# Optimization experiments

Hardware: AMD Instinct MI355X
Metric: run time of the kernel (lower is better)

Reference implementation:

```python
import jax, jax.numpy as jnp
import numpy as np
import math

N, C3, T = 32, 192, 2048  # C3 = 3 * head_dim

def setup_inputs() -> dict:
    key = jax.random.key(0)
    qkv = jax.random.normal(key, (N, C3, T), dtype=jnp.float32)
    return {"qkv": qkv}

def reference(qkv):
    ch = qkv.shape[1] // 3
    q, k, v = jnp.split(qkv, 3, axis=1)              # each [N, C, T]
    scale = 1.0 / math.sqrt(math.sqrt(ch))           # applied to both q and k
    # [N, T, T] attention scores
    weight = jnp.einsum('bct,bcs->bts', q * scale, k * scale)
    weight = jax.nn.softmax(weight.astype(jnp.float32), axis=-1).astype(qkv.dtype)
    # [N, C, T] output
    return jnp.einsum('bts,bcs->bct', weight, v)
```

## Files before the change

kernel.cpp:

```cpp
#include <hip/hip_runtime.h>

#define T_DIM 2048
#define NB 32

#define QT_OFF 0
#define KB_OFF 4194304
#define VB_OFF 8388608

typedef _Float16 half8 __attribute__((ext_vector_type(8)));
typedef _Float16 half4 __attribute__((ext_vector_type(4)));
typedef float f32x16 __attribute__((ext_vector_type(16)));
typedef float f32x4 __attribute__((ext_vector_type(4)));

#define ZERO16 (f32x16){0.f,0.f,0.f,0.f,0.f,0.f,0.f,0.f,0.f,0.f,0.f,0.f,0.f,0.f,0.f,0.f}

__global__ __launch_bounds__(256) void prepass(const float* __restrict__ qkv,
                                               _Float16* __restrict__ ws) {
  const int ttile = blockIdx.x;
  const int b = blockIdx.y;
  const int type = blockIdx.z;
  const int t0 = ttile * 64;
  __shared__ float Ls[64][65];

  const int tid = threadIdx.x;
  const int cc = tid >> 4;
  const int tt = (tid & 15) << 2;
  const float QS = 0.125f * 1.4426950408889634f;
  const float* src = qkv + ((size_t)b * 192 + type * 64) * T_DIM;
#pragma unroll
  for (int p = 0; p < 4; ++p) {
    const int c = p * 16 + cc;
    float4 v = *(const float4*)&src[(size_t)c * T_DIM + t0 + tt];
    if (type == 0) { v.x *= QS; v.y *= QS; v.z *= QS; v.w *= QS; }
    Ls[c][tt] = v.x; Ls[c][tt + 1] = v.y; Ls[c][tt + 2] = v.z; Ls[c][tt + 3] = v.w;
  }
  __syncthreads();

  if (type == 0) {
    const int t = tid >> 2, cg = (tid & 3) * 16;
    half8 h0, h1;
#pragma unroll
    for (int j = 0; j < 8; ++j) h0[j] = (_Float16)Ls[cg + j][t];
#pragma unroll
    for (int j = 0; j < 8; ++j) h1[j] = (_Float16)Ls[cg + 8 + j][t];
    _Float16* dst = ws + QT_OFF + ((size_t)b * T_DIM + t0 + t) * 64 + cg;
    *(half8*)dst = h0;
    *(half8*)(dst + 8) = h1;
  } else if (type == 1) {
    const int f = tid >> 6, h = (tid >> 5) & 1, s31 = tid & 31;
#pragma unroll
    for (int sbl = 0; sbl < 2; ++sbl) {
      const int sb = (t0 >> 5) + sbl;
      half8 hv;
#pragma unroll
      for (int j = 0; j < 8; ++j) hv[j] = (_Float16)Ls[f * 16 + h * 8 + j][sbl * 32 + s31];
      _Float16* dst = ws + KB_OFF + ((size_t)b * 64 + sb) * 2048 + f * 512 + h * 256 + s31 * 8;
      *(half8*)dst = hv;
    }
  } else {
#pragma unroll
    for (int p = 0; p < 2; ++p) {
      const int g = p * 256 + tid;
      const int sgl = g >> 6, c = g & 63;
      half8 hv;
#pragma unroll
      for (int j = 0; j < 8; ++j) hv[j] = (_Float16)Ls[c][sgl * 8 + j];
      _Float16* dst = ws + VB_OFF + (((size_t)b * 256 + (t0 >> 3) + sgl) * 64 + c) * 8;
      *(half8*)dst = hv;
    }
  }
}

__global__ __launch_bounds__(256, 4) void qkv_main(const _Float16* __restrict__ ws,
                                                   float* __restrict__ out) {
  const int tid = threadIdx.x;
  const int wave = tid >> 6, lane = tid & 63;
  const int l31 = lane & 31, h = lane >> 5;
  const int qh = wave & 1;
  const int kh = wave >> 1;
  const int b = blockIdx.x & 31;
  const int qg = blockIdx.x >> 5;
  const int t0 = qg * 64 + qh * 32;

  __shared__ float cl[2][64][36];

  const _Float16* kbase = ws + KB_OFF + (size_t)b * 131072 + (size_t)kh * 65536;
  const _Float16* vbase = ws + VB_OFF + (size_t)b * 131072 + (size_t)kh * 65536;

  const _Float16* qp = ws + QT_OFF + ((size_t)b * T_DIM + t0 + l31) * 64 + h * 8;
  half8 bq[4];
#pragma unroll
  for (int f = 0; f < 4; ++f) bq[f] = *(const half8*)(qp + f * 16);

  f32x16 o0 = ZERO16, o1 = ZERO16;
  float lp = 0.f;

  const _Float16* kp = kbase + h * 256 + l31 * 8;
  const _Float16* vp = vbase + l31 * 8 + h * 4;

  half8 ak0 = *(const half8*)(kp);
  half8 ak1 = *(const half8*)(kp + 512);
  half8 ak2 = *(const half8*)(kp + 1024);
  half8 ak3 = *(const half8*)(kp + 1536);

  for (int sb = 0; sb < 32; ++sb) {
    const size_t off = (size_t)(sb + 1 < 32 ? sb + 1 : sb) * 2048;
    half8 nk0 = *(const half8*)(kp + off);
    half8 nk1 = *(const half8*)(kp + off + 512);
    half8 nk2 = *(const half8*)(kp + off + 1024);
    half8 nk3 = *(const half8*)(kp + off + 1536);
    const _Float16* vpi = vp + (size_t)sb * 2048;
    half4 bv[8];
#pragma unroll
    for (int g = 0; g < 4; ++g) {
      bv[2 * g] = *(const half4*)(vpi + g * 512);
      bv[2 * g + 1] = *(const half4*)(vpi + g * 512 + 256);
    }

    f32x16 s = ZERO16;
    s = __builtin_amdgcn_mfma_f32_32x32x16_f16(ak0, bq[0], s, 0, 0, 0);
    s = __builtin_amdgcn_mfma_f32_32x32x16_f16(ak1, bq[1], s, 0, 0, 0);
    s = __builtin_amdgcn_mfma_f32_32x32x16_f16(ak2, bq[2], s, 0, 0, 0);
    s = __builtin_amdgcn_mfma_f32_32x32x16_f16(ak3, bq[3], s, 0, 0, 0);

    half4 ap[4];
    float lp0 = 0.f, lp1 = 0.f;
#pragma unroll
    for (int g = 0; g < 4; ++g) {
      const float e0 = __builtin_amdgcn_exp2f(s[4 * g + 0]);
      const float e1 = __builtin_amdgcn_exp2f(s[4 * g + 1]);
      const float e2 = __builtin_amdgcn_exp2f(s[4 * g + 2]);
      const float e3 = __builtin_amdgcn_exp2f(s[4 * g + 3]);
      lp0 += e0 + e1;
      lp1 += e2 + e3;
      ap[g] = (half4){(_Float16)e0, (_Float16)e1, (_Float16)e2, (_Float16)e3};
    }
    lp += lp0 + lp1;

#pragma unroll
    for (int g = 0; g < 4; ++g) {
      o0 = __builtin_amdgcn_mfma_f32_32x32x8f16(ap[g], bv[2 * g], o0, 0, 0, 0);
      o1 = __builtin_amdgcn_mfma_f32_32x32x8f16(ap[g], bv[2 * g + 1], o1, 0, 0, 0);
    }

    ak0 = nk0; ak1 = nk1; ak2 = nk2; ak3 = nk3;
  }

  if (kh == 1) {
#pragma unroll
    for (int g = 0; g < 4; ++g) {
      *(f32x4*)&cl[qh][lane][g * 4] =
          (f32x4){o0[4 * g], o0[4 * g + 1], o0[4 * g + 2], o0[4 * g + 3]};
      *(f32x4*)&cl[qh][lane][16 + g * 4] =
          (f32x4){o1[4 * g], o1[4 * g + 1], o1[4 * g + 2], o1[4 * g + 3]};
    }
    cl[qh][lane][32] = lp;
  }
  __syncthreads();
  if (kh == 0) {
#pragma unroll
    for (int g = 0; g < 4; ++g) {
      const f32x4 p0 = *(const f32x4*)&cl[qh][lane][g * 4];
      const f32x4 p1 = *(const f32x4*)&cl[qh][lane][16 + g * 4];
#pragma unroll
      for (int j = 0; j < 4; ++j) {
        o0[4 * g + j] += p0[j];
        o1[4 * g + j] += p1[j];
      }
    }
    lp += cl[qh][lane][32];
    const float lf = lp + __shfl_xor(lp, 32);
    const float linv = 1.0f / lf;
    float* ob = out + (size_t)b * 64 * T_DIM + t0;
#pragma unroll
    for (int g = 0; g < 4; ++g) {
      f32x4 r0, r1;
#pragma unroll
      for (int j = 0; j < 4; ++j) {
        const float il = __shfl(linv, g * 8 + h * 4 + j);
        r0[j] = o0[g * 4 + j] * il;
        r1[j] = o1[g * 4 + j] * il;
      }
      const int q = g * 8 + h * 4;
      *(f32x4*)&ob[(size_t)l31 * T_DIM + q] = r0;
      *(f32x4*)&ob[(size_t)(32 + l31) * T_DIM + q] = r1;
    }
  }
}

extern "C" void kernel_launch(void* const* d_in, const int* in_sizes, int n_in,
                              void* d_out, int out_size, void* d_ws, size_t ws_size,
                              hipStream_t stream) {
  const float* qkv = (const float*)d_in[0];
  float* out = (float*)d_out;
  _Float16* ws = (_Float16*)d_ws;
  hipLaunchKernelGGL(prepass, dim3(32, 32, 3), dim3(256), 0, stream, qkv, ws);
  hipLaunchKernelGGL(qkv_main, dim3(1024), dim3(256), 0, stream, ws, out);
}
```

Measured before the change: 141.5 us.

## Use K=16 MFMA for PV product with cross-half shuffles and prefetch V

Replaces the eight 32x32x8 f16 MFMAs in the P·V product with four 32x32x16 MFMAs per iteration. The probability fragments are regrouped across lane halves with xor-32 shuffles so they match the wider K layout, and V is read as half8 with a new offset pattern. V loads are also double-buffered alongside K one iteration ahead, and the loop is unrolled by two. This cuts MFMA issue count and overlaps V loads with compute, at the cost of extra shuffles and higher register pressure under the occupancy-4 launch bound.

```diff
diff --git a/kernel.cpp b/kernel.cpp
--- a/kernel.cpp
+++ b/kernel.cpp
@@ -11,8 +11,16 @@
 typedef _Float16 half4 __attribute__((ext_vector_type(4)));
 typedef float f32x16 __attribute__((ext_vector_type(16)));
 typedef float f32x4 __attribute__((ext_vector_type(4)));
+typedef int i32x2 __attribute__((ext_vector_type(2)));
 
 #define ZERO16 (f32x16){0.f,0.f,0.f,0.f,0.f,0.f,0.f,0.f,0.f,0.f,0.f,0.f,0.f,0.f,0.f,0.f}
+
+__device__ __forceinline__ half4 shflx32(half4 v) {
+  i32x2 i = __builtin_bit_cast(i32x2, v);
+  i.x = __shfl_xor(i.x, 32);
+  i.y = __shfl_xor(i.y, 32);
+  return __builtin_bit_cast(half4, i);
+}
 
 __global__ __launch_bounds__(256) void prepass(const float* __restrict__ qkv,
                                                _Float16* __restrict__ ws) {
@@ -96,32 +104,34 @@
   float lp = 0.f;
 
   const _Float16* kp = kbase + h * 256 + l31 * 8;
-  const _Float16* vp = vbase + l31 * 8 + h * 4;
-
-  half8 ak0 = *(const half8*)(kp);
-  half8 ak1 = *(const half8*)(kp + 512);
-  half8 ak2 = *(const half8*)(kp + 1024);
-  half8 ak3 = *(const half8*)(kp + 1536);
-
+  const _Float16* vp = vbase + h * 512 + l31 * 8;
+
+  half8 ak[2][4], av[2][4];
+#pragma unroll
+  for (int f = 0; f < 4; ++f) ak[0][f] = *(const half8*)(kp + f * 512);
+  av[0][0] = *(const half8*)(vp);
+  av[0][1] = *(const half8*)(vp + 256);
+  av[0][2] = *(const half8*)(vp + 1024);
+  av[0][3] = *(const half8*)(vp + 1280);
+
+#pragma unroll 2
   for (int sb = 0; sb < 32; ++sb) {
-    const size_t off = (size_t)(sb + 1 < 32 ? sb + 1 : sb) * 2048;
-    half8 nk0 = *(const half8*)(kp + off);
-    half8 nk1 = *(const half8*)(kp + off + 512);
-    half8 nk2 = *(const half8*)(kp + off + 1024);
-    half8 nk3 = *(const half8*)(kp + off + 1536);
-    const _Float16* vpi = vp + (size_t)sb * 2048;
-    half4 bv[8];
-#pragma unroll
-    for (int g = 0; g < 4; ++g) {
-      bv[2 * g] = *(const half4*)(vpi + g * 512);
-      bv[2 * g + 1] = *(const half4*)(vpi + g * 512 + 256);
-    }
+    const int cur = sb & 1, nxt = cur ^ 1;
+    const size_t noff = (size_t)(sb + 1 < 32 ? sb + 1 : sb) * 2048;
+    ak[nxt][0] = *(const half8*)(kp + noff);
+    ak[nxt][1] = *(const half8*)(kp + noff + 512);
+    ak[nxt][2] = *(const half8*)(kp + noff + 1024);
+    ak[nxt][3] = *(const half8*)(kp + noff + 1536);
+    av[nxt][0] = *(const half8*)(vp + noff);
+    av[nxt][1] = *(const half8*)(vp + noff + 256);
+    av[nxt][2] = *(const half8*)(vp + noff + 1024);
+    av[nxt][3] = *(const half8*)(vp + noff + 1280);
 
     f32x16 s = ZERO16;
-    s = __builtin_amdgcn_mfma_f32_32x32x16_f16(ak0, bq[0], s, 0, 0, 0);
-    s = __builtin_amdgcn_mfma_f32_32x32x16_f16(ak1, bq[1], s, 0, 0, 0);
-    s = __builtin_amdgcn_mfma_f32_32x32x16_f16(ak2, bq[2], s, 0, 0, 0);
-    s = __builtin_amdgcn_mfma_f32_32x32x16_f16(ak3, bq[3], s, 0, 0, 0);
+    s = __builtin_amdgcn_mfma_f32_32x32x16_f16(ak[cur][0], bq[0], s, 0, 0, 0);
+    s = __builtin_amdgcn_mfma_f32_32x32x16_f16(ak[cur][1], bq[1], s, 0, 0, 0);
+    s = __builtin_amdgcn_mfma_f32_32x32x16_f16(ak[cur][2], bq[2], s, 0, 0, 0);
+    s = __builtin_amdgcn_mfma_f32_32x32x16_f16(ak[cur][3], bq[3], s, 0, 0, 0);
 
     half4 ap[4];
     float lp0 = 0.f, lp1 = 0.f;
@@ -138,12 +148,15 @@
     lp += lp0 + lp1;
 
 #pragma unroll
-    for (int g = 0; g < 4; ++g) {
-      o0 = __builtin_amdgcn_mfma_f32_32x32x8f16(ap[g], bv[2 * g], o0, 0, 0, 0);
-      o1 = __builtin_amdgcn_mfma_f32_32x32x8f16(ap[g], bv[2 * g + 1], o1, 0, 0, 0);
-    }
-
-    ak0 = nk0; ak1 = nk1; ak2 = nk2; ak3 = nk3;
+    for (int gp = 0; gp < 2; ++gp) {
+      const half4 a0 = ap[2 * gp], a1 = ap[2 * gp + 1];
+      const half4 sw0 = shflx32(a0), sw1 = shflx32(a1);
+      const half4 lo = h ? sw1 : a0;
+      const half4 hi = h ? a1 : sw0;
+      const half8 a16 = __builtin_shufflevector(lo, hi, 0, 1, 2, 3, 4, 5, 6, 7);
+      o0 = __builtin_amdgcn_mfma_f32_32x32x16_f16(a16, av[cur][2 * gp], o0, 0, 0, 0);
+      o1 = __builtin_amdgcn_mfma_f32_32x32x16_f16(a16, av[cur][2 * gp + 1], o1, 0, 0, 0);
+    }
   }
 
   if (kh == 1) {
```

Measured after the change: 152.2 us. +7.6%, slower.
